# Optimization experiments

Measured on AMD Instinct MI355X. Metric: run time of the kernel, lower is better.

The kernel has to match this reference:

```python
import jax, jax.numpy as jnp
import numpy as np

B, L, INP, HID, NCLS = 512, 256, 300, 256, 5  # trees, leaves/tree, embed dim, hidden, classes


def setup_inputs() -> dict:
    key = jax.random.key(0)
    ks = jax.random.split(key, 7)
    s_in = 1.0 / np.sqrt(INP).astype(np.float32)
    s_h = 1.0 / np.sqrt(HID).astype(np.float32)
    # W_leaf order: [inp_gate, out_gate, upd_gate]
    # W_nl order:  [inp_ln, inp_rn, fo_l_l, fo_l_r, fo_r_l, fo_r_r, out_ln, out_rn, upd_ln, upd_rn]
    return {
        "embeddings": jax.random.normal(ks[0], (B, L, INP), jnp.float32),
        "W_leaf": jax.random.uniform(ks[1], (3, INP, HID), jnp.float32, -s_in, s_in),
        "b_leaf": jax.random.uniform(ks[2], (3, HID), jnp.float32, -s_in, s_in),
        "W_nl": jax.random.uniform(ks[3], (10, HID, HID), jnp.float32, -s_h, s_h),
        "b_nl": jax.random.uniform(ks[4], (10, HID), jnp.float32, -s_h, s_h),
        "W_out": jax.random.uniform(ks[5], (HID, NCLS), jnp.float32, -s_h, s_h),
        "b_out": jax.random.uniform(ks[6], (NCLS,), jnp.float32, -s_h, s_h),
    }


def reference(embeddings, W_leaf, b_leaf, W_nl, b_nl, W_out, b_out):
    sig, tanh = jax.nn.sigmoid, jnp.tanh
    # ---- leaf nodes (depth 0), batched over all B*L leaves ----
    pre = jnp.einsum('bli,gih->blgh', embeddings, W_leaf) + b_leaf  # [B,L,3,H]
    i_g = sig(pre[:, :, 0])
    o_g = sig(pre[:, :, 1])
    u_g = tanh(pre[:, :, 2])
    c = i_g * u_g                      # [B,L,H]
    h = o_g * sig(c)                   # note: leaf uses sigmoid(cell), as in torch code
    logits = [jnp.einsum('bnh,hc->bnc', h, W_out) + b_out]
    # ---- internal nodes, level-synchronous ----
    Wl = W_nl[0::2]                    # [5,H,H] acting on left hidden
    Wr = W_nl[1::2]                    # [5,H,H] acting on right hidden
    bb = b_nl[0::2] + b_nl[1::2]       # [5,H]
    n = L
    while n > 1:
        lc, rc = c[:, 0::2], c[:, 1::2]
        lh, rh = h[:, 0::2], h[:, 1::2]
        pre = (jnp.einsum('bnh,ghk->bngk', lh, Wl)
               + jnp.einsum('bnh,ghk->bngk', rh, Wr) + bb)  # [B,n/2,5,H]
        inp_g = sig(pre[:, :, 0])
        fol_g = sig(pre[:, :, 1])
        for_g = sig(pre[:, :, 2])
        out_g = sig(pre[:, :, 3])
        upd_g = tanh(pre[:, :, 4])
        c = inp_g * upd_g + fol_g * lc + for_g * rc
        h = out_g * tanh(c)
        logits.append(jnp.einsum('bnh,hc->bnc', h, W_out) + b_out)
        n //= 2
    # per-node class scores for all 2L-1 nodes (leaves first, root last)
    return jnp.concatenate(logits, axis=1)  # [B, 2L-1, NCLS]
```

## Files before the change

kernel.cpp:

```cpp
#include <hip/hip_runtime.h>
#include <hip/hip_bf16.h>


#define HID 256

typedef __attribute__((ext_vector_type(8))) short short8;
typedef __attribute__((ext_vector_type(4))) float f32x4;
typedef __attribute__((ext_vector_type(4))) unsigned short ushort4v;

__device__ __forceinline__ float rcpf(float x) { return __builtin_amdgcn_rcpf(x); }
__device__ __forceinline__ float sigf(float x) { return rcpf(1.0f + __expf(-x)); }
__device__ __forceinline__ float tanhf_(float x) { return 2.0f * rcpf(1.0f + __expf(-2.0f * x)) - 1.0f; }
__device__ __forceinline__ unsigned short f2bf(float f) {
    __hip_bfloat16 b = __float2bfloat16(f);
    return *(unsigned short*)&b;
}
__device__ __forceinline__ void gload_lds16(const void* g, void* l) {
    __builtin_amdgcn_global_load_lds(
        (const __attribute__((address_space(1))) unsigned int*)g,
        (__attribute__((address_space(3))) unsigned int*)l, 16, 0, 0);
}
template <int N> __device__ __forceinline__ void waitcnt_vm() {
    if constexpr (N == 0)       asm volatile("s_waitcnt vmcnt(0)" ::: "memory");
    else if constexpr (N == 9)  asm volatile("s_waitcnt vmcnt(9)" ::: "memory");
    else if constexpr (N == 10) asm volatile("s_waitcnt vmcnt(10)" ::: "memory");
    else                        asm volatile("s_waitcnt vmcnt(0)" ::: "memory");
}

template <int NG, int FG, int NCB, int K, bool LEAF>
__global__ __launch_bounds__(256, 2) void gemm_mid(
    const unsigned short* __restrict__ A,
    const unsigned short* __restrict__ BT,
    const float* __restrict__ bias,
    const float* __restrict__ cprev,
    float* __restrict__ cout,
    unsigned short* __restrict__ hout,
    const float* __restrict__ W_out,
    float* __restrict__ out,
    int log2n, int off)
{
    constexpr int CW   = FG * 16;
    constexpr int GW   = 2 * CW;
    constexpr int BN   = NG * GW;
    constexpr int NK   = K / 64;
    constexpr int NBW  = BN / 32;
    constexpr int L    = 4 + NBW;
    constexpr int NF   = NG * FG;
    constexpr int ABUF = 128 * 128;
    constexpr int BBUF = BN * 128;
    constexpr int BUF  = ABUF + BBUF;
    constexpr int HS   = GW + 4;

    __shared__ char smem[2 * BUF];

    const int t = threadIdx.x;
    const int lane = t & 63;
    const int w = t >> 6;
    const int wm = w >> 1, wn = w & 1;

    const int bid = blockIdx.x;
    const int xcd = bid & 7;
    const int slot = bid >> 3;
    const int cb = slot % NCB;
    const int row0 = ((slot / NCB) * 8 + xcd) * 128;

    const int l3 = lane >> 3;
    const unsigned int swsrc = (unsigned int)(((lane & 7) ^ l3) * 16);
    unsigned int a_src[4];
    unsigned int b_src[NBW];
#pragma unroll
    for (int q = 0; q < 4; ++q)
        a_src[q] = (unsigned int)(row0 + (w * 4 + q) * 8 + l3) * (K * 2) + swsrc;
#pragma unroll
    for (int q = 0; q < NBW; ++q)
        b_src[q] = (unsigned int)(cb * BN + (w * NBW + q) * 8 + l3) * (K * 2) + swsrc;

    const int swz0 = ((lane >> 4) ^ (lane & 7)) * 16;
    const int swz1 = (((lane >> 4) + 4) ^ (lane & 7)) * 16;
    const int aoff = (wm * 64 + (lane & 15)) * 128;
    const int boff = (wn * CW + (lane & 15)) * 128;

    f32x4 acc[4][NF] = {};

    auto STAGE = [&](int buf, int kt) {
        char* As = smem + buf * BUF;
        char* Bs = As + ABUF;
        const unsigned int k0b = (unsigned int)kt * 128;
#pragma unroll
        for (int q = 0; q < 4; ++q)
            gload_lds16((const char*)A + (size_t)(a_src[q] + k0b),
                        As + (w * 4 + q) * 1024);
#pragma unroll
        for (int q = 0; q < NBW; ++q)
            gload_lds16((const char*)BT + (size_t)(b_src[q] + k0b),
                        Bs + (w * NBW + q) * 1024);
    };

    STAGE(0, 0);
    STAGE(1, 1);

#pragma unroll
    for (int kt = 0; kt < NK; ++kt) {
        const int cur = kt & 1;
        if (kt + 1 < NK) waitcnt_vm<L>(); else waitcnt_vm<0>();
        __builtin_amdgcn_s_barrier();
        const char* As = smem + cur * BUF;
        const char* Bs = As + ABUF;
#pragma unroll
        for (int ks = 0; ks < 2; ++ks) {
            const int sw = ks ? swz1 : swz0;
            short8 a[4], b[NF];
#pragma unroll
            for (int mf = 0; mf < 4; ++mf)
                a[mf] = *(const short8*)(As + aoff + mf * 2048 + sw);
#pragma unroll
            for (int g = 0; g < NG; ++g)
#pragma unroll
                for (int fc = 0; fc < FG; ++fc)
                    b[g * FG + fc] = *(const short8*)(Bs + g * (GW * 128) +
                                                      fc * 2048 + boff + sw);
            __builtin_amdgcn_s_setprio(1);
#pragma unroll
            for (int f = 0; f < NF; ++f)
#pragma unroll
                for (int mf = 0; mf < 4; ++mf)
                    acc[mf][f] = __builtin_amdgcn_mfma_f32_16x16x32_bf16(
                        a[mf], b[f], acc[mf][f], 0, 0, 0);
            __builtin_amdgcn_s_setprio(0);
        }
        asm volatile("s_waitcnt lgkmcnt(0)" ::: "memory");
        __builtin_amdgcn_sched_barrier(0);
        __builtin_amdgcn_s_barrier();
        if (kt + 2 < NK) STAGE(cur, kt + 2);
    }

    float* hs = (float*)smem;
    float* Wt = (float*)(smem + 128 * HS * 4);
    for (int i = t; i < 5 * GW; i += 256) {
        int cls = i / GW, c2 = i % GW;
        Wt[i] = W_out[(cb * GW + c2) * 5 + cls];
    }

#pragma unroll
    for (int mf = 0; mf < 4; ++mf) {
#pragma unroll
        for (int j = 0; j < 4; ++j) {
            const int rl = wm * 64 + mf * 16 + ((lane >> 4) << 2) + j;
            const int r = row0 + rl;
#pragma unroll
            for (int fc = 0; fc < FG; ++fc) {
                const int cl = wn * CW + fc * 16 + (lane & 15);
                const int c = cb * GW + cl;
                float cv, hv;
                if constexpr (LEAF) {
                    float p0 = acc[mf][0 * FG + fc][j] + bias[c];
                    float p1 = acc[mf][1 * FG + fc][j] + bias[256 + c];
                    float p2 = acc[mf][2 * FG + fc][j] + bias[512 + c];
                    cv = sigf(p0) * tanhf_(p2);
                    hv = sigf(p1) * sigf(cv);
                } else {
                    float p0 = acc[mf][0 * FG + fc][j] + bias[c];
                    float p1 = acc[mf][1 * FG + fc][j] + bias[256 + c];
                    float p2 = acc[mf][2 * FG + fc][j] + bias[512 + c];
                    float p3 = acc[mf][3 * FG + fc][j] + bias[768 + c];
                    float p4 = acc[mf][4 * FG + fc][j] + bias[1024 + c];
                    float lc = cprev[(size_t)r * 512 + c];
                    float rc = cprev[(size_t)r * 512 + 256 + c];
                    cv = sigf(p0) * tanhf_(p4) + sigf(p1) * lc + sigf(p2) * rc;
                    hv = sigf(p3) * tanhf_(cv);
                }
                cout[(size_t)r * 256 + c] = cv;
                hout[(size_t)r * 256 + c] = f2bf(hv);
                hs[rl * HS + cl] = hv;
            }
        }
    }
    __syncthreads();

    const int nmask = (1 << log2n) - 1;
    for (int idx = t; idx < 128 * 5; idx += 256) {
        int rl = idx / 5, cls = idx - rl * 5;
        float s = 0.f;
#pragma unroll
        for (int q = 0; q < GW / 4; ++q) {
            const float4 h4 = *(const float4*)(hs + rl * HS + q * 4);
            const float4 w4 = *(const float4*)(Wt + cls * GW + q * 4);
            s += h4.x * w4.x + h4.y * w4.y + h4.z * w4.z + h4.w * w4.w;
        }
        int rg = row0 + rl;
        int b = rg >> log2n, jj = rg & nmask;
        atomicAdd(out + ((size_t)b * 511 + off + jj) * 5 + cls, s);
    }
}

template <int NG, int K>
__global__ __launch_bounds__(256, 3) void gemm_small(
    const unsigned short* __restrict__ A,
    const unsigned short* __restrict__ BT,
    const float* __restrict__ bias,
    const float* __restrict__ cprev,
    float* __restrict__ cout,
    unsigned short* __restrict__ hout,
    const float* __restrict__ W_out,
    float* __restrict__ out,
    int log2n, int off)
{
    constexpr int CS  = 32;
    constexpr int BN  = NG * CS;
    constexpr int NK  = K / 64;
    constexpr int NBW = BN / 32;
    constexpr int ABUF = 128 * 128;

    __shared__ char smem[2 * ABUF + BN * 128];
    char* Bs = smem + 2 * ABUF;

    const int t = threadIdx.x;
    const int lane = t & 63;
    const int w = t >> 6;
    const int wm = w >> 1, wn = w & 1;
    const int cb = blockIdx.x;
    const int row0 = blockIdx.y * 128;

    const int l3 = lane >> 3;
    const unsigned int swsrc = (unsigned int)(((lane & 7) ^ l3) * 16);
    unsigned int a_src[4];
    unsigned int b_src[NBW];
#pragma unroll
    for (int q = 0; q < 4; ++q)
        a_src[q] = (unsigned int)(row0 + (w * 4 + q) * 8 + l3) * (K * 2) + swsrc;
#pragma unroll
    for (int q = 0; q < NBW; ++q)
        b_src[q] = (unsigned int)(cb * BN + (w * NBW + q) * 8 + l3) * (K * 2) + swsrc;

    const int swz0 = ((lane >> 4) ^ (lane & 7)) * 16;
    const int swz1 = (((lane >> 4) + 4) ^ (lane & 7)) * 16;
    const int aoff = (wm * 64 + (lane & 15)) * 128;
    const int boff = (wn * 16 + (lane & 15)) * 128;

    f32x4 acc[4][NG] = {};

    auto STAGE_A = [&](int buf, int kt) {
        char* As = smem + buf * ABUF;
        const unsigned int k0b = (unsigned int)kt * 128;
#pragma unroll
        for (int q = 0; q < 4; ++q)
            gload_lds16((const char*)A + (size_t)(a_src[q] + k0b),
                        As + (w * 4 + q) * 1024);
    };
    auto STAGE_B = [&](int kt) {
        const unsigned int k0b = (unsigned int)kt * 128;
#pragma unroll
        for (int q = 0; q < NBW; ++q)
            gload_lds16((const char*)BT + (size_t)(b_src[q] + k0b),
                        Bs + (w * NBW + q) * 1024);
    };

    STAGE_A(0, 0);
    STAGE_B(0);
    asm volatile("s_waitcnt vmcnt(0)" ::: "memory");
    __builtin_amdgcn_s_barrier();
    asm volatile("" ::: "memory");

#pragma unroll
    for (int kt = 0; kt < NK; ++kt) {
        const int cur = kt & 1;
        if (kt + 1 < NK) STAGE_A(cur ^ 1, kt + 1);
        const char* As = smem + cur * ABUF;
#pragma unroll
        for (int ks = 0; ks < 2; ++ks) {
            const int sw = ks ? swz1 : swz0;
            short8 a[4];
#pragma unroll
            for (int mf = 0; mf < 4; ++mf)
                a[mf] = *(const short8*)(As + aoff + mf * 2048 + sw);
#pragma unroll
            for (int g = 0; g < NG; ++g) {
                short8 b = *(const short8*)(Bs + g * (CS * 128) + boff + sw);
#pragma unroll
                for (int mf = 0; mf < 4; ++mf)
                    acc[mf][g] = __builtin_amdgcn_mfma_f32_16x16x32_bf16(
                        a[mf], b, acc[mf][g], 0, 0, 0);
            }
        }
        asm volatile("" ::: "memory");
        __builtin_amdgcn_s_barrier();
        asm volatile("" ::: "memory");
        if (kt + 1 < NK) {
            STAGE_B(kt + 1);
            asm volatile("s_waitcnt vmcnt(0)" ::: "memory");
        }
        __builtin_amdgcn_s_barrier();
        asm volatile("" ::: "memory");
    }

    float* hs = (float*)smem;
    float* Wt = (float*)(smem + 128 * 36 * 4);
    for (int i = t; i < 5 * CS; i += 256) {
        int cls = i / CS, c2 = i % CS;
        Wt[i] = W_out[(cb * CS + c2) * 5 + cls];
    }

#pragma unroll
    for (int mf = 0; mf < 4; ++mf) {
#pragma unroll
        for (int j = 0; j < 4; ++j) {
            const int rl = wm * 64 + mf * 16 + ((lane >> 4) << 2) + j;
            const int r = row0 + rl;
            const int cl = wn * 16 + (lane & 15);
            const int c = cb * CS + cl;
            float p0 = acc[mf][0][j] + bias[c];
            float p1 = acc[mf][1][j] + bias[256 + c];
            float p2 = acc[mf][2][j] + bias[512 + c];
            float p3 = acc[mf][3][j] + bias[768 + c];
            float p4 = acc[mf][4][j] + bias[1024 + c];
            float lc = cprev[(size_t)r * 512 + c];
            float rc = cprev[(size_t)r * 512 + 256 + c];
            float cv = sigf(p0) * tanhf_(p4) + sigf(p1) * lc + sigf(p2) * rc;
            float hv = sigf(p3) * tanhf_(cv);
            cout[(size_t)r * 256 + c] = cv;
            hout[(size_t)r * 256 + c] = f2bf(hv);
            hs[rl * 36 + cl] = hv;
        }
    }
    __syncthreads();

    const int nmask = (1 << log2n) - 1;
    for (int idx = t; idx < 128 * 5; idx += 256) {
        int rl = idx / 5, cls = idx - rl * 5;
        float s = 0.f;
#pragma unroll
        for (int q = 0; q < CS / 4; ++q) {
            const float4 h4 = *(const float4*)(hs + rl * 36 + q * 4);
            const float4 w4 = *(const float4*)(Wt + cls * CS + q * 4);
            s += h4.x * w4.x + h4.y * w4.y + h4.z * w4.z + h4.w * w4.w;
        }
        int rg = row0 + rl;
        int b = rg >> log2n, jj = rg & nmask;
        atomicAdd(out + ((size_t)b * 511 + off + jj) * 5 + cls, s);
    }
}

__global__ __launch_bounds__(256) void prep_weights(
    const float* __restrict__ W_leaf, const float* __restrict__ W_nl,
    const float* __restrict__ b_nl, const float* __restrict__ b_out,
    unsigned short* __restrict__ BleafT,
    unsigned short* __restrict__ BlevT,
    float* __restrict__ bb, float* __restrict__ out)
{
    const int T1 = 768 * 320, T2 = 1280 * 512, T3 = 5 * 256, T4 = 261632 * 5;
    for (int idx = blockIdx.x * 256 + threadIdx.x; idx < T1 + T2 + T3 + T4;
         idx += gridDim.x * 256) {
        if (idx < T1) {
            int colp = idx / 320, k = idx % 320;
            int cbv = colp / 192, rem = colp % 192;
            int g = rem >> 6, cl = rem & 63;
            int c = cbv * 64 + cl;
            float v = (k < 300) ? W_leaf[((size_t)g * 300 + k) * 256 + c] : 0.0f;
            BleafT[(size_t)colp * 320 + k] = f2bf(v);
        } else if (idx < T1 + T2) {
            int i2 = idx - T1;
            int colp = i2 / 512, k = i2 % 512;
            int cb8 = colp / 160, rem = colp % 160;
            int g = rem >> 5, cl = rem & 31;
            int c = cb8 * 32 + cl;
            float v = W_nl[((size_t)(2 * g + (k >= 256)) * 256 + (k & 255)) * 256 + c];
            BlevT[(size_t)colp * 512 + k] = f2bf(v);
        } else if (idx < T1 + T2 + T3) {
            int i3 = idx - T1 - T2;
            bb[i3] = b_nl[(size_t)(i3 >> 8) * 512 + (i3 & 255)] +
                     b_nl[(size_t)(i3 >> 8) * 512 + 256 + (i3 & 255)];
        } else {
            int i4 = idx - T1 - T2 - T3;
            out[i4] = b_out[i4 % 5];
        }
    }
}

__global__ __launch_bounds__(256) void emb_to_bf16(
    const float* __restrict__ emb, unsigned short* __restrict__ embB)
{
    const int total = 131072 * 80;
    for (int idx = blockIdx.x * 256 + threadIdx.x; idx < total;
         idx += gridDim.x * 256) {
        int r = idx / 80, q = idx % 80;
        ushort4v o;
        if (q < 75) {
            const float4 v = *(const float4*)(emb + (size_t)r * 300 + q * 4);
            o.x = f2bf(v.x); o.y = f2bf(v.y); o.z = f2bf(v.z); o.w = f2bf(v.w);
        } else {
            o.x = 0; o.y = 0; o.z = 0; o.w = 0;
        }
        *(ushort4v*)(embB + (size_t)r * 320 + q * 4) = o;
    }
}

extern "C" void kernel_launch(void* const* d_in, const int* in_sizes, int n_in,
                              void* d_out, int out_size, void* d_ws, size_t ws_size,
                              hipStream_t stream) {
    const float* emb    = (const float*)d_in[0];
    const float* W_leaf = (const float*)d_in[1];
    const float* b_leaf = (const float*)d_in[2];
    const float* W_nl   = (const float*)d_in[3];
    const float* b_nl   = (const float*)d_in[4];
    const float* W_out  = (const float*)d_in[5];
    const float* b_out  = (const float*)d_in[6];
    float* out = (float*)d_out;

    char* ws = (char*)d_ws;
    unsigned short* embB   = (unsigned short*)(ws);
    unsigned short* BleafT = (unsigned short*)(ws + 83886080);
    unsigned short* BlevT  = (unsigned short*)(ws + 84377600);
    float*          bb     = (float*)(ws + 85688320);
    float*          cA     = (float*)(ws + 85693440);
    unsigned short* hA     = (unsigned short*)(ws + 219911168);
    float*          cB     = (float*)(ws + 287020032);
    unsigned short* hB     = (unsigned short*)(ws + 354128896);

    prep_weights<<<2048, 256, 0, stream>>>(W_leaf, W_nl, b_nl, b_out,
                                           BleafT, BlevT, bb, out);
    emb_to_bf16<<<2048, 256, 0, stream>>>(emb, embB);

    gemm_mid<3, 2, 4, 320, true><<<4096, 256, 0, stream>>>(
        embB, BleafT, b_leaf, nullptr, cA, hA, W_out, out, 8, 0);

    const unsigned short* hp = hA;
    const float* cp = cA;
    int off = 256;
    for (int lev = 1; lev <= 8; ++lev) {
        int log2n = 8 - lev;
        int n = 1 << log2n;
        int M = 512 * n;
        float* cd = (lev & 1) ? cB : cA;
        unsigned short* hd = (lev & 1) ? hB : hA;
        if (M >= 16384) {
            gemm_mid<5, 1, 8, 512, false><<<(M / 128) * 8, 256, 0, stream>>>(
                hp, BlevT, bb, cp, cd, hd, W_out, out, log2n, off);
        } else {
            gemm_small<5, 512><<<dim3(8, M / 128), 256, 0, stream>>>(
                hp, BlevT, bb, cp, cd, hd, W_out, out, log2n, off);
        }
        cp = cd;
        hp = hd;
        off += n;
    }
}
```

Before: 467.2 us.

## Move per-level logits out of GEMM epilogues into one atomic-free kernel

Drops the shared-memory logits reduction and the atomicAdd scatter from every GEMM epilogue. Each level's bf16 hidden states now go to their own region of the workspace (reusing the bf16 embedding buffer after the leaf GEMM). A single final kernel then computes all node logits with a warp-shuffle reduction, adds the bias and writes each output once, so the separate output bias initialisation is gone. This removes millions of atomics and an extra block barrier per GEMM. In exchange it adds a full extra read of every hidden state, and logits are now computed from bf16 rather than fp32 hidden values.

```diff
diff --git a/kernel.cpp b/kernel.cpp
--- a/kernel.cpp
+++ b/kernel.cpp
@@ -11,6 +11,9 @@
 __device__ __forceinline__ float rcpf(float x) { return __builtin_amdgcn_rcpf(x); }
 __device__ __forceinline__ float sigf(float x) { return rcpf(1.0f + __expf(-x)); }
 __device__ __forceinline__ float tanhf_(float x) { return 2.0f * rcpf(1.0f + __expf(-2.0f * x)) - 1.0f; }
+__device__ __forceinline__ float bf2f(unsigned short u) {
+    union { unsigned int i; float f; } v; v.i = ((unsigned int)u) << 16; return v.f;
+}
 __device__ __forceinline__ unsigned short f2bf(float f) {
     __hip_bfloat16 b = __float2bfloat16(f);
     return *(unsigned short*)&b;
@@ -34,10 +37,7 @@
     const float* __restrict__ bias,
     const float* __restrict__ cprev,
     float* __restrict__ cout,
-    unsigned short* __restrict__ hout,
-    const float* __restrict__ W_out,
-    float* __restrict__ out,
-    int log2n, int off)
+    unsigned short* __restrict__ hout)
 {
     constexpr int CW   = FG * 16;
     constexpr int GW   = 2 * CW;
@@ -49,7 +49,6 @@
     constexpr int ABUF = 128 * 128;
     constexpr int BBUF = BN * 128;
     constexpr int BUF  = ABUF + BBUF;
-    constexpr int HS   = GW + 4;
 
     __shared__ char smem[2 * BUF];
 
@@ -132,13 +131,6 @@
         __builtin_amdgcn_sched_barrier(0);
         __builtin_amdgcn_s_barrier();
         if (kt + 2 < NK) STAGE(cur, kt + 2);
-    }
-
-    float* hs = (float*)smem;
-    float* Wt = (float*)(smem + 128 * HS * 4);
-    for (int i = t; i < 5 * GW; i += 256) {
-        int cls = i / GW, c2 = i % GW;
-        Wt[i] = W_out[(cb * GW + c2) * 5 + cls];
     }
 
 #pragma unroll
@@ -171,25 +163,8 @@
                 }
                 cout[(size_t)r * 256 + c] = cv;
                 hout[(size_t)r * 256 + c] = f2bf(hv);
-                hs[rl * HS + cl] = hv;
             }
         }
-    }
-    __syncthreads();
-
-    const int nmask = (1 << log2n) - 1;
-    for (int idx = t; idx < 128 * 5; idx += 256) {
-        int rl = idx / 5, cls = idx - rl * 5;
-        float s = 0.f;
-#pragma unroll
-        for (int q = 0; q < GW / 4; ++q) {
-            const float4 h4 = *(const float4*)(hs + rl * HS + q * 4);
-            const float4 w4 = *(const float4*)(Wt + cls * GW + q * 4);
-            s += h4.x * w4.x + h4.y * w4.y + h4.z * w4.z + h4.w * w4.w;
-        }
-        int rg = row0 + rl;
-        int b = rg >> log2n, jj = rg & nmask;
-        atomicAdd(out + ((size_t)b * 511 + off + jj) * 5 + cls, s);
     }
 }
 
@@ -200,10 +175,7 @@
     const float* __restrict__ bias,
     const float* __restrict__ cprev,
     float* __restrict__ cout,
-    unsigned short* __restrict__ hout,
-    const float* __restrict__ W_out,
-    float* __restrict__ out,
-    int log2n, int off)
+    unsigned short* __restrict__ hout)
 {
     constexpr int CS  = 32;
     constexpr int BN  = NG * CS;
@@ -293,13 +265,6 @@
         asm volatile("" ::: "memory");
     }
 
-    float* hs = (float*)smem;
-    float* Wt = (float*)(smem + 128 * 36 * 4);
-    for (int i = t; i < 5 * CS; i += 256) {
-        int cls = i / CS, c2 = i % CS;
-        Wt[i] = W_out[(cb * CS + c2) * 5 + cls];
-    }
-
 #pragma unroll
     for (int mf = 0; mf < 4; ++mf) {
 #pragma unroll
@@ -307,7 +272,7 @@
             const int rl = wm * 64 + mf * 16 + ((lane >> 4) << 2) + j;
             const int r = row0 + rl;
             const int cl = wn * 16 + (lane & 15);
-            const int c = cb * CS + cl;
+            const int c = cb * 32 + cl;
             float p0 = acc[mf][0][j] + bias[c];
             float p1 = acc[mf][1][j] + bias[256 + c];
             float p2 = acc[mf][2][j] + bias[512 + c];
@@ -319,36 +284,80 @@
             float hv = sigf(p3) * tanhf_(cv);
             cout[(size_t)r * 256 + c] = cv;
             hout[(size_t)r * 256 + c] = f2bf(hv);
-            hs[rl * 36 + cl] = hv;
-        }
-    }
+        }
+    }
+}
+
+__global__ __launch_bounds__(256) void logits_all(
+    const unsigned short* __restrict__ hA,
+    const unsigned short* __restrict__ hRest,
+    const float* __restrict__ W_out, const float* __restrict__ b_out,
+    float* __restrict__ out)
+{
+    __shared__ float Ws[HID * 5];
+    __shared__ float bs[5];
+    const int t = threadIdx.x;
+    for (int i = t; i < HID * 5; i += 256) Ws[i] = W_out[i];
+    if (t < 5) bs[t] = b_out[t];
     __syncthreads();
 
-    const int nmask = (1 << log2n) - 1;
-    for (int idx = t; idx < 128 * 5; idx += 256) {
-        int rl = idx / 5, cls = idx - rl * 5;
-        float s = 0.f;
-#pragma unroll
-        for (int q = 0; q < CS / 4; ++q) {
-            const float4 h4 = *(const float4*)(hs + rl * 36 + q * 4);
-            const float4 w4 = *(const float4*)(Wt + cls * CS + q * 4);
-            s += h4.x * w4.x + h4.y * w4.y + h4.z * w4.z + h4.w * w4.w;
-        }
-        int rg = row0 + rl;
-        int b = rg >> log2n, jj = rg & nmask;
-        atomicAdd(out + ((size_t)b * 511 + off + jj) * 5 + cls, s);
+    const int part = t & 15;
+    const int rl = t >> 4;
+    const int R = blockIdx.x * 16 + rl;
+
+    const unsigned short* h = (R < 131072)
+        ? hA + (size_t)R * HID
+        : hRest + (size_t)(R - 131072) * HID;
+
+    float a0 = 0.f, a1 = 0.f, a2 = 0.f, a3 = 0.f, a4 = 0.f;
+#pragma unroll
+    for (int i = 0; i < 2; ++i) {
+        short8 hv = *(const short8*)(h + part * 16 + i * 8);
+#pragma unroll
+        for (int e = 0; e < 8; ++e) {
+            float f = bf2f((unsigned short)hv[e]);
+            int c = part * 16 + i * 8 + e;
+            a0 = fmaf(f, Ws[c * 5 + 0], a0);
+            a1 = fmaf(f, Ws[c * 5 + 1], a1);
+            a2 = fmaf(f, Ws[c * 5 + 2], a2);
+            a3 = fmaf(f, Ws[c * 5 + 3], a3);
+            a4 = fmaf(f, Ws[c * 5 + 4], a4);
+        }
+    }
+#pragma unroll
+    for (int m = 8; m >= 1; m >>= 1) {
+        a0 += __shfl_xor(a0, m);
+        a1 += __shfl_xor(a1, m);
+        a2 += __shfl_xor(a2, m);
+        a3 += __shfl_xor(a3, m);
+        a4 += __shfl_xor(a4, m);
+    }
+    if (part == 0) {
+        unsigned int V = 262144u - (unsigned int)R;
+        int lev = 17 - (31 - __clz(V - 1));
+        int start = 262144 - (1 << (18 - lev));
+        int local = R - start;
+        int nb = 8 - lev;
+        int b = local >> nb, j = local & ((1 << nb) - 1);
+        int off = 512 - (1 << (9 - lev));
+        size_t o = ((size_t)b * 511 + off + j) * 5;
+        out[o + 0] = a0 + bs[0];
+        out[o + 1] = a1 + bs[1];
+        out[o + 2] = a2 + bs[2];
+        out[o + 3] = a3 + bs[3];
+        out[o + 4] = a4 + bs[4];
     }
 }
 
 __global__ __launch_bounds__(256) void prep_weights(
     const float* __restrict__ W_leaf, const float* __restrict__ W_nl,
-    const float* __restrict__ b_nl, const float* __restrict__ b_out,
+    const float* __restrict__ b_nl,
     unsigned short* __restrict__ BleafT,
     unsigned short* __restrict__ BlevT,
-    float* __restrict__ bb, float* __restrict__ out)
+    float* __restrict__ bb)
 {
-    const int T1 = 768 * 320, T2 = 1280 * 512, T3 = 5 * 256, T4 = 261632 * 5;
-    for (int idx = blockIdx.x * 256 + threadIdx.x; idx < T1 + T2 + T3 + T4;
+    const int T1 = 768 * 320, T2 = 1280 * 512, T3 = 5 * 256;
+    for (int idx = blockIdx.x * 256 + threadIdx.x; idx < T1 + T2 + T3;
          idx += gridDim.x * 256) {
         if (idx < T1) {
             int colp = idx / 320, k = idx % 320;
@@ -365,13 +374,10 @@
             int c = cb8 * 32 + cl;
             float v = W_nl[((size_t)(2 * g + (k >= 256)) * 256 + (k & 255)) * 256 + c];
             BlevT[(size_t)colp * 512 + k] = f2bf(v);
-        } else if (idx < T1 + T2 + T3) {
+        } else {
             int i3 = idx - T1 - T2;
             bb[i3] = b_nl[(size_t)(i3 >> 8) * 512 + (i3 & 255)] +
                      b_nl[(size_t)(i3 >> 8) * 512 + 256 + (i3 & 255)];
-        } else {
-            int i4 = idx - T1 - T2 - T3;
-            out[i4] = b_out[i4 % 5];
         }
     }
 }
@@ -408,39 +414,39 @@
 
     char* ws = (char*)d_ws;
     unsigned short* embB   = (unsigned short*)(ws);
+    unsigned short* hRest  = (unsigned short*)(ws);
     unsigned short* BleafT = (unsigned short*)(ws + 83886080);
     unsigned short* BlevT  = (unsigned short*)(ws + 84377600);
     float*          bb     = (float*)(ws + 85688320);
     float*          cA     = (float*)(ws + 85693440);
     unsigned short* hA     = (unsigned short*)(ws + 219911168);
     float*          cB     = (float*)(ws + 287020032);
-    unsigned short* hB     = (unsigned short*)(ws + 354128896);
-
-    prep_weights<<<2048, 256, 0, stream>>>(W_leaf, W_nl, b_nl, b_out,
-                                           BleafT, BlevT, bb, out);
+
+    prep_weights<<<1024, 256, 0, stream>>>(W_leaf, W_nl, b_nl, BleafT, BlevT, bb);
     emb_to_bf16<<<2048, 256, 0, stream>>>(emb, embB);
 
     gemm_mid<3, 2, 4, 320, true><<<4096, 256, 0, stream>>>(
-        embB, BleafT, b_leaf, nullptr, cA, hA, W_out, out, 8, 0);
+        embB, BleafT, b_leaf, nullptr, cA, hA);
 
     const unsigned short* hp = hA;
     const float* cp = cA;
-    int off = 256;
+    size_t hoff = 0;
     for (int lev = 1; lev <= 8; ++lev) {
-        int log2n = 8 - lev;
-        int n = 1 << log2n;
+        int n = 1 << (8 - lev);
         int M = 512 * n;
         float* cd = (lev & 1) ? cB : cA;
-        unsigned short* hd = (lev & 1) ? hB : hA;
+        unsigned short* hd = hRest + hoff;
         if (M >= 16384) {
             gemm_mid<5, 1, 8, 512, false><<<(M / 128) * 8, 256, 0, stream>>>(
-                hp, BlevT, bb, cp, cd, hd, W_out, out, log2n, off);
+                hp, BlevT, bb, cp, cd, hd);
         } else {
             gemm_small<5, 512><<<dim3(8, M / 128), 256, 0, stream>>>(
-                hp, BlevT, bb, cp, cd, hd, W_out, out, log2n, off);
+                hp, BlevT, bb, cp, cd, hd);
         }
         cp = cd;
         hp = hd;
-        off += n;
-    }
-}
+        hoff += (size_t)M * HID;
+    }
+
+    logits_all<<<261632 / 16, 256, 0, stream>>>(hA, hRest, W_out, b_out, out);
+}
```

Result: slower. 546.3 us (+16.9%).
